# Performance work log

Hardware: AMD Instinct MI355X
Metric: run time of the kernel (lower is better)

The kernel has to match this reference:

```python
import jax, jax.numpy as jnp
import numpy as np

N = 500_000      # total nodes across all graphs in batch
B = 128          # batch_size (number of graphs)
S = 128          # state_size
D = 128          # aggregated_size


def setup_inputs() -> dict:
    key = jax.random.key(0)
    k1, k2, k3, k4, k5, k6 = jax.random.split(key, 6)
    nodes = jax.random.normal(k1, (N, S), dtype=jnp.float32)
    owner_masks = jax.random.randint(k2, (B, N), 0, 2, dtype=jnp.int32)
    # Linear params (torch Linear: y = x @ W.T + b); store W as [in, out] for x @ W
    scale = 1.0 / np.sqrt(S)
    Wt = jax.random.uniform(k3, (S, D), jnp.float32, -scale, scale)
    bt = jax.random.uniform(k4, (D,), jnp.float32, -scale, scale)
    Wg = jax.random.uniform(k5, (S, D), jnp.float32, -scale, scale)
    bg = jax.random.uniform(k6, (D,), jnp.float32, -scale, scale)
    return {"nodes": nodes, "owner_masks": owner_masks,
            "Wt": Wt, "bt": bt, "Wg": Wg, "bg": bg}


def reference(nodes, owner_masks, Wt, bt, Wg, bg):
    # gates = sigmoid(nodes @ Wg + bg)   [N, D]
    gates = jax.nn.sigmoid(nodes @ Wg + bg)
    # data = nodes @ Wt + bt             [N, D]
    data = nodes @ Wt + bt
    # pooled = owner_masks.float() @ (data * gates)   [B, D]
    return owner_masks.astype(jnp.float32) @ (data * gates)
```

## Files before the change

### kernel.cpp

```cpp
#include <hip/hip_runtime.h>


#define NTOT   500000
#define NBLK   512
#define NCHUNK 15625

typedef __attribute__((ext_vector_type(8))) unsigned short ushort8;
typedef __bf16 bf16x8 __attribute__((ext_vector_type(8)));
typedef __attribute__((ext_vector_type(4))) float f32x4;

static __device__ __forceinline__ unsigned short f2bf(float f) {
  unsigned int u = __float_as_uint(f);
  u += 0x7fffu + ((u >> 16) & 1u);
  return (unsigned short)(u >> 16);
}

static __device__ __forceinline__ unsigned long long pack4(unsigned short a, unsigned short b,
                                                           unsigned short c, unsigned short d) {
  return (unsigned long long)a | ((unsigned long long)b << 16) |
         ((unsigned long long)c << 32) | ((unsigned long long)d << 48);
}

template <bool ATOMIC>
__global__ __launch_bounds__(256, 2)
void agg_main(const float* __restrict__ nodes, const int* __restrict__ masks,
              const float* __restrict__ Wt, const float* __restrict__ bt,
              const float* __restrict__ Wg, const float* __restrict__ bg,
              float* __restrict__ outp) {
  __shared__ __align__(16) unsigned short nodes_s[32][136];
  __shared__ __align__(16) unsigned short mask_s[128][40];
  __shared__ __align__(16) unsigned short vt_s[128][40];

  const int tid = threadIdx.x;
  const int lane = tid & 63;
  const int w = tid >> 6;
  const int q = lane >> 4;
  const int r = lane & 15;

  bf16x8 Wf[2][4][2];
  float btr[2], bgr[2];
#pragma unroll
  for (int nt = 0; nt < 2; ++nt) {
    const int d = w * 32 + nt * 16 + r;
    btr[nt] = bt[d];
    bgr[nt] = bg[d];
#pragma unroll
    for (int ks = 0; ks < 4; ++ks) {
      ushort8 ft, fg;
#pragma unroll
      for (int j = 0; j < 8; ++j) {
        const int k = ks * 32 + q * 8 + j;
        ft[j] = f2bf(Wt[k * 128 + d]);
        fg[j] = f2bf(Wg[k * 128 + d]);
      }
      Wf[0][ks][nt] = __builtin_bit_cast(bf16x8, ft);
      Wf[1][ks][nt] = __builtin_bit_cast(bf16x8, fg);
    }
  }

  f32x4 acc[4][4];
  const f32x4 fzero = {0.f, 0.f, 0.f, 0.f};
#pragma unroll
  for (int i = 0; i < 4; ++i)
#pragma unroll
    for (int j = 0; j < 4; ++j) acc[i][j] = fzero;

  const int bid = blockIdx.x;
  const int c0 = (int)(((long long)bid * NCHUNK) / NBLK);
  const int c1 = (int)(((long long)(bid + 1) * NCHUNK) / NBLK);

  float4 nf[4];
  int4 mi[4];
  auto issue = [&](int c) {
    const int k0 = c * 32;
#pragma unroll
    for (int it = 0; it < 4; ++it) {
      const int flat = it * 256 + tid;
      const int nrow = flat >> 5, nc4 = flat & 31;
      nf[it] = *(const float4*)(nodes + (size_t)(k0 + nrow) * 128 + nc4 * 4);
      const int mrow = flat >> 3, mc4 = flat & 7;
      mi[it] = *(const int4*)(masks + (size_t)mrow * NTOT + k0 + mc4 * 4);
    }
  };

  if (c0 < c1) issue(c0);

  for (int c = c0; c < c1; ++c) {
    __syncthreads();
#pragma unroll
    for (int it = 0; it < 4; ++it) {
      const int flat = it * 256 + tid;
      const int nrow = flat >> 5, nc4 = flat & 31;
      *(unsigned long long*)&nodes_s[nrow][nc4 * 4] =
          pack4(f2bf(nf[it].x), f2bf(nf[it].y), f2bf(nf[it].z), f2bf(nf[it].w));
      const int mrow = flat >> 3, mc4 = flat & 7;
      *(unsigned long long*)&mask_s[mrow][mc4 * 4] =
          pack4(f2bf((float)mi[it].x), f2bf((float)mi[it].y),
                f2bf((float)mi[it].z), f2bf((float)mi[it].w));
    }
    __syncthreads();
    if (c + 1 < c1) issue(c + 1);

    f32x4 aD[2][2], aG[2][2];
#pragma unroll
    for (int i = 0; i < 2; ++i)
#pragma unroll
      for (int j = 0; j < 2; ++j) { aD[i][j] = fzero; aG[i][j] = fzero; }
#pragma unroll
    for (int ks = 0; ks < 4; ++ks) {
      bf16x8 a0 = *(const bf16x8*)&nodes_s[r][ks * 32 + q * 8];
      bf16x8 a1 = *(const bf16x8*)&nodes_s[16 + r][ks * 32 + q * 8];
#pragma unroll
      for (int nt = 0; nt < 2; ++nt) {
        aD[0][nt] = __builtin_amdgcn_mfma_f32_16x16x32_bf16(a0, Wf[0][ks][nt], aD[0][nt], 0, 0, 0);
        aD[1][nt] = __builtin_amdgcn_mfma_f32_16x16x32_bf16(a1, Wf[0][ks][nt], aD[1][nt], 0, 0, 0);
        aG[0][nt] = __builtin_amdgcn_mfma_f32_16x16x32_bf16(a0, Wf[1][ks][nt], aG[0][nt], 0, 0, 0);
        aG[1][nt] = __builtin_amdgcn_mfma_f32_16x16x32_bf16(a1, Wf[1][ks][nt], aG[1][nt], 0, 0, 0);
      }
    }

#pragma unroll
    for (int mt = 0; mt < 2; ++mt)
#pragma unroll
      for (int nt = 0; nt < 2; ++nt) {
        const int d = w * 32 + nt * 16 + r;
        unsigned short t[4];
#pragma unroll
        for (int reg = 0; reg < 4; ++reg) {
          const float x = aD[mt][nt][reg] + btr[nt];
          const float g = aG[mt][nt][reg] + bgr[nt];
          t[reg] = f2bf(x / (1.f + __expf(-g)));
        }
        *(unsigned long long*)&vt_s[d][mt * 16 + q * 4] = pack4(t[0], t[1], t[2], t[3]);
      }
    __syncthreads();

    const int mb = (w >> 1) * 64, nb = (w & 1) * 64;
    bf16x8 bfr[4];
#pragma unroll
    for (int nt = 0; nt < 4; ++nt)
      bfr[nt] = *(const bf16x8*)&vt_s[nb + nt * 16 + r][q * 8];
#pragma unroll
    for (int mt = 0; mt < 4; ++mt) {
      bf16x8 af = *(const bf16x8*)&mask_s[mb + mt * 16 + r][q * 8];
#pragma unroll
      for (int nt = 0; nt < 4; ++nt)
        acc[mt][nt] = __builtin_amdgcn_mfma_f32_16x16x32_bf16(af, bfr[nt], acc[mt][nt], 0, 0, 0);
    }
  }

#pragma unroll
  for (int mt = 0; mt < 4; ++mt)
#pragma unroll
    for (int nt = 0; nt < 4; ++nt)
#pragma unroll
      for (int reg = 0; reg < 4; ++reg) {
        const int b = (w >> 1) * 64 + mt * 16 + q * 4 + reg;
        const int d = (w & 1) * 64 + nt * 16 + r;
        if (ATOMIC)
          atomicAdd(&outp[b * 128 + d], acc[mt][nt][reg]);
        else
          outp[(size_t)bid * 16384 + b * 128 + d] = acc[mt][nt][reg];
      }
}

__global__ __launch_bounds__(256)
void agg_reduce(const float* __restrict__ part, float* __restrict__ out) {
  const int gid = blockIdx.x * 256 + threadIdx.x;
  const int i = gid & 16383;
  const int grp = gid >> 14;
  const float* p = part + (size_t)grp * 64 * 16384 + i;
  float s = 0.f;
#pragma unroll 8
  for (int g = 0; g < 64; ++g) s += p[(size_t)g * 16384];
  atomicAdd(&out[i], s);
}

extern "C" void kernel_launch(void* const* d_in, const int* in_sizes, int n_in,
                              void* d_out, int out_size, void* d_ws, size_t ws_size,
                              hipStream_t stream) {
  const float* nodes = (const float*)d_in[0];
  const int*   masks = (const int*)d_in[1];
  const float* Wt    = (const float*)d_in[2];
  const float* bt    = (const float*)d_in[3];
  const float* Wg    = (const float*)d_in[4];
  const float* bg    = (const float*)d_in[5];
  float* out = (float*)d_out;

  hipMemsetAsync(d_out, 0, (size_t)out_size * sizeof(float), stream);

  const size_t need = (size_t)NBLK * 16384 * sizeof(float);
  if (ws_size >= need) {
    agg_main<false><<<NBLK, 256, 0, stream>>>(nodes, masks, Wt, bt, Wg, bg, (float*)d_ws);
    agg_reduce<<<512, 256, 0, stream>>>((const float*)d_ws, out);
  } else {
    agg_main<true><<<NBLK, 256, 0, stream>>>(nodes, masks, Wt, bt, Wg, bg, out);
  }
}
```

Baseline: 521.8 us.

## Precompute per-block mask bitmaps via ballot and drop a per-chunk barrier

Each block first reads its whole 1024-node slice of the int32 owner masks and packs it into bitmaps in shared memory using wave ballots. In the main loop it builds bf16 0/1 A-fragments directly from those bits, instead of staging bf16-converted masks per chunk. The pooling MFMA is repartitioned so each wave covers all 128 graphs for its own 32 output features. Because a wave only reads back the gated values it wrote itself, one __syncthreads per chunk can be removed. The grid shrinks to 500 blocks so the chunk split lines up with the bitmap, and the reduce kernel is adjusted to match. The trade-off is an up-front mask load phase that is not overlapped with compute.

Result: slower. 562.5 us (+7.8%).

```diff
diff --git a/kernel.cpp b/kernel.cpp
--- a/kernel.cpp
+++ b/kernel.cpp
@@ -2,23 +2,29 @@
 
 
 #define NTOT   500000
-#define NBLK   512
+#define NBLK   500
 #define NCHUNK 15625
+
+typedef unsigned long long u64;
+typedef unsigned int u32;
 
 typedef __attribute__((ext_vector_type(8))) unsigned short ushort8;
 typedef __bf16 bf16x8 __attribute__((ext_vector_type(8)));
 typedef __attribute__((ext_vector_type(4))) float f32x4;
 
 static __device__ __forceinline__ unsigned short f2bf(float f) {
-  unsigned int u = __float_as_uint(f);
+  u32 u = __float_as_uint(f);
   u += 0x7fffu + ((u >> 16) & 1u);
   return (unsigned short)(u >> 16);
 }
 
-static __device__ __forceinline__ unsigned long long pack4(unsigned short a, unsigned short b,
-                                                           unsigned short c, unsigned short d) {
-  return (unsigned long long)a | ((unsigned long long)b << 16) |
-         ((unsigned long long)c << 32) | ((unsigned long long)d << 48);
+static __device__ __forceinline__ u64 pack4(unsigned short a, unsigned short b,
+                                            unsigned short c, unsigned short d) {
+  return (u64)a | ((u64)b << 16) | ((u64)c << 32) | ((u64)d << 48);
+}
+
+static __device__ __forceinline__ u32 bits2bf2(u32 byte, int j) {
+  return ((byte >> j) & 1u ? 0x3F80u : 0u) | ((byte >> (j + 1)) & 1u ? 0x3F800000u : 0u);
 }
 
 template <bool ATOMIC>
@@ -28,7 +34,7 @@
               const float* __restrict__ Wg, const float* __restrict__ bg,
               float* __restrict__ outp) {
   __shared__ __align__(16) unsigned short nodes_s[32][136];
-  __shared__ __align__(16) unsigned short mask_s[128][40];
+  __shared__ __align__(16) u64 bits[128][17];
   __shared__ __align__(16) unsigned short vt_s[128][40];
 
   const int tid = threadIdx.x;
@@ -37,6 +43,12 @@
   const int q = lane >> 4;
   const int r = lane & 15;
 
+  const int bid = blockIdx.x;
+  const int c0 = (int)(((long long)bid * NCHUNK) / NBLK);
+  const int c1 = (int)(((long long)(bid + 1) * NCHUNK) / NBLK);
+  const int nch = c1 - c0;
+  const int n0 = c0 * 32;
+
   bf16x8 Wf[2][4][2];
   float btr[2], bgr[2];
 #pragma unroll
@@ -58,48 +70,68 @@
     }
   }
 
-  f32x4 acc[4][4];
+  {
+    const int row0 = w * 32;
+    int cur[32], nxt[32];
+#pragma unroll
+    for (int k = 0; k < 32; ++k)
+      cur[k] = masks[(size_t)(row0 + k) * NTOT + n0 + lane];
+#pragma unroll
+    for (int g = 0; g < 16; ++g) {
+      if (g < 15) {
+#pragma unroll
+        for (int k = 0; k < 32; ++k)
+          nxt[k] = masks[(size_t)(row0 + k) * NTOT + n0 + (g + 1) * 64 + lane];
+      }
+      u64 v = 0;
+#pragma unroll
+      for (int k = 0; k < 32; ++k) {
+        u64 bl = __ballot(cur[k] != 0);
+        if (lane == k) v = bl;
+      }
+      if (lane < 32) bits[row0 + lane][g] = v;
+      if (g < 15) {
+#pragma unroll
+        for (int k = 0; k < 32; ++k) cur[k] = nxt[k];
+      }
+    }
+  }
+
+  f32x4 acc[8][2];
   const f32x4 fzero = {0.f, 0.f, 0.f, 0.f};
 #pragma unroll
-  for (int i = 0; i < 4; ++i)
-#pragma unroll
-    for (int j = 0; j < 4; ++j) acc[i][j] = fzero;
-
-  const int bid = blockIdx.x;
-  const int c0 = (int)(((long long)bid * NCHUNK) / NBLK);
-  const int c1 = (int)(((long long)(bid + 1) * NCHUNK) / NBLK);
+  for (int i = 0; i < 8; ++i) {
+    acc[i][0] = fzero;
+    acc[i][1] = fzero;
+  }
 
   float4 nf[4];
-  int4 mi[4];
-  auto issue = [&](int c) {
-    const int k0 = c * 32;
+  auto issue = [&](int cloc) {
+    const int k0 = n0 + cloc * 32;
 #pragma unroll
     for (int it = 0; it < 4; ++it) {
       const int flat = it * 256 + tid;
       const int nrow = flat >> 5, nc4 = flat & 31;
       nf[it] = *(const float4*)(nodes + (size_t)(k0 + nrow) * 128 + nc4 * 4);
-      const int mrow = flat >> 3, mc4 = flat & 7;
-      mi[it] = *(const int4*)(masks + (size_t)mrow * NTOT + k0 + mc4 * 4);
     }
   };
 
-  if (c0 < c1) issue(c0);
-
-  for (int c = c0; c < c1; ++c) {
-    __syncthreads();
+  issue(0);
+  __syncthreads();
+
+  const u32* bitw = (const u32*)bits;
+
+  for (int c = 0; c < nch; ++c) {
+    if (c) __syncthreads();
 #pragma unroll
     for (int it = 0; it < 4; ++it) {
       const int flat = it * 256 + tid;
       const int nrow = flat >> 5, nc4 = flat & 31;
-      *(unsigned long long*)&nodes_s[nrow][nc4 * 4] =
+      *(u64*)&nodes_s[nrow][nc4 * 4] =
           pack4(f2bf(nf[it].x), f2bf(nf[it].y), f2bf(nf[it].z), f2bf(nf[it].w));
-      const int mrow = flat >> 3, mc4 = flat & 7;
-      *(unsigned long long*)&mask_s[mrow][mc4 * 4] =
-          pack4(f2bf((float)mi[it].x), f2bf((float)mi[it].y),
-                f2bf((float)mi[it].z), f2bf((float)mi[it].w));
     }
     __syncthreads();
-    if (c + 1 < c1) issue(c + 1);
+    if (c + 1 < nch) issue(c + 1);
 
     f32x4 aD[2][2], aG[2][2];
 #pragma unroll
@@ -131,32 +163,35 @@
           const float g = aG[mt][nt][reg] + bgr[nt];
           t[reg] = f2bf(x / (1.f + __expf(-g)));
         }
-        *(unsigned long long*)&vt_s[d][mt * 16 + q * 4] = pack4(t[0], t[1], t[2], t[3]);
-      }
-    __syncthreads();
-
-    const int mb = (w >> 1) * 64, nb = (w & 1) * 64;
-    bf16x8 bfr[4];
-#pragma unroll
-    for (int nt = 0; nt < 4; ++nt)
-      bfr[nt] = *(const bf16x8*)&vt_s[nb + nt * 16 + r][q * 8];
-#pragma unroll
-    for (int mt = 0; mt < 4; ++mt) {
-      bf16x8 af = *(const bf16x8*)&mask_s[mb + mt * 16 + r][q * 8];
-#pragma unroll
-      for (int nt = 0; nt < 4; ++nt)
-        acc[mt][nt] = __builtin_amdgcn_mfma_f32_16x16x32_bf16(af, bfr[nt], acc[mt][nt], 0, 0, 0);
-    }
-  }
-
-#pragma unroll
-  for (int mt = 0; mt < 4; ++mt)
-#pragma unroll
-    for (int nt = 0; nt < 4; ++nt)
+        *(u64*)&vt_s[d][mt * 16 + q * 4] = pack4(t[0], t[1], t[2], t[3]);
+      }
+
+    bf16x8 bfr[2];
+#pragma unroll
+    for (int nt = 0; nt < 2; ++nt)
+      bfr[nt] = *(const bf16x8*)&vt_s[w * 32 + nt * 16 + r][q * 8];
+#pragma unroll
+    for (int mt = 0; mt < 8; ++mt) {
+      const u32 dw = bitw[(mt * 16 + r) * 34 + c];
+      const u32 byte = (dw >> (q * 8)) & 0xffu;
+      u32 p0 = bits2bf2(byte, 0), p1 = bits2bf2(byte, 2);
+      u32 p2 = bits2bf2(byte, 4), p3 = bits2bf2(byte, 6);
+      u32 af[4] = {p0, p1, p2, p3};
+      bf16x8 a = __builtin_bit_cast(bf16x8, *(ushort8*)af);
+#pragma unroll
+      for (int nt = 0; nt < 2; ++nt)
+        acc[mt][nt] = __builtin_amdgcn_mfma_f32_16x16x32_bf16(a, bfr[nt], acc[mt][nt], 0, 0, 0);
+    }
+  }
+
+#pragma unroll
+  for (int mt = 0; mt < 8; ++mt)
+#pragma unroll
+    for (int nt = 0; nt < 2; ++nt)
 #pragma unroll
       for (int reg = 0; reg < 4; ++reg) {
-        const int b = (w >> 1) * 64 + mt * 16 + q * 4 + reg;
-        const int d = (w & 1) * 64 + nt * 16 + r;
+        const int b = mt * 16 + q * 4 + reg;
+        const int d = w * 32 + nt * 16 + r;
         if (ATOMIC)
           atomicAdd(&outp[b * 128 + d], acc[mt][nt][reg]);
         else
@@ -169,10 +204,10 @@
   const int gid = blockIdx.x * 256 + threadIdx.x;
   const int i = gid & 16383;
   const int grp = gid >> 14;
-  const float* p = part + (size_t)grp * 64 * 16384 + i;
+  const float* p = part + (size_t)grp * 125 * 16384 + i;
   float s = 0.f;
-#pragma unroll 8
-  for (int g = 0; g < 64; ++g) s += p[(size_t)g * 16384];
+#pragma unroll 5
+  for (int g = 0; g < 125; ++g) s += p[(size_t)g * 16384];
   atomicAdd(&out[i], s);
 }
 
@@ -192,7 +227,7 @@
   const size_t need = (size_t)NBLK * 16384 * sizeof(float);
   if (ws_size >= need) {
     agg_main<false><<<NBLK, 256, 0, stream>>>(nodes, masks, Wt, bt, Wg, bg, (float*)d_ws);
-    agg_reduce<<<512, 256, 0, stream>>>((const float*)d_ws, out);
+    agg_reduce<<<256, 256, 0, stream>>>((const float*)d_ws, out);
   } else {
     agg_main<true><<<NBLK, 256, 0, stream>>>(nodes, masks, Wt, bt, Wg, bg, out);
   }
```
